# Kernel tuning notes

Measured on AMD Instinct MI355X. Metric: run time of the kernel, lower is better.

Reference implementation:

```python
import jax, jax.numpy as jnp
import numpy as np

N = 50000   # nodes
E = 800000  # edges
G = 64      # graphs in batch
D = 128     # num_input
H = 128     # num_hidden
O = 10      # num_output


def _linear_params(key, fan_in, fan_out):
    k1, k2 = jax.random.split(key)
    s = 1.0 / np.sqrt(fan_in)
    W = jax.random.uniform(k1, (fan_out, fan_in), jnp.float32, -s, s)
    b = jax.random.uniform(k2, (fan_out,), jnp.float32, -s, s)
    return W, b


def setup_inputs() -> dict:
    key = jax.random.key(0)
    ks = jax.random.split(key, 12)
    x = jax.random.normal(ks[0], (N, D), jnp.float32)
    edge_index = jax.random.randint(ks[1], (2, E), 0, N, dtype=jnp.int32).astype(jnp.int64)
    batch = jnp.sort(jax.random.randint(ks[2], (N,), 0, G, dtype=jnp.int32)).astype(jnp.int64)

    W_rel1, b_rel1 = _linear_params(ks[3], D, H)
    W_root1, _ = _linear_params(ks[4], D, H)
    W_rel2, b_rel2 = _linear_params(ks[5], H, H)
    W_root2, _ = _linear_params(ks[6], H, H)
    W_rel3, b_rel3 = _linear_params(ks[7], H, H)
    W_root3, _ = _linear_params(ks[8], H, H)
    W1, b1 = _linear_params(ks[9], 2 * H, 128)
    W2, b2 = _linear_params(ks[10], 128, 64)
    W3, b3 = _linear_params(ks[11], 64, O)

    return dict(x=x, edge_index=edge_index, batch=batch,
                W_rel1=W_rel1, b_rel1=b_rel1, W_root1=W_root1,
                W_rel2=W_rel2, b_rel2=b_rel2, W_root2=W_root2,
                W_rel3=W_rel3, b_rel3=b_rel3, W_root3=W_root3,
                W1=W1, b1=b1, W2=W2, b2=b2, W3=W3, b3=b3)


def _graph_conv(x, src, dst, W_rel, b_rel, W_root):
    # PyG GraphConv (aggr='add'): out_i = W_rel @ sum_{j->i} x_j + b_rel + W_root @ x_i
    agg = jax.ops.segment_sum(x[src], dst, num_segments=N)  # [N, d]
    return agg @ W_rel.T + b_rel + x @ W_root.T


def _pool(x, batch):
    # concat(global_max_pool, global_mean_pool) -> [G, 2d]
    mx = jax.ops.segment_max(x, batch, num_segments=G)
    mx = jnp.where(jnp.isfinite(mx), mx, 0.0)  # guard empty segments
    sm = jax.ops.segment_sum(x, batch, num_segments=G)
    cnt = jax.ops.segment_sum(jnp.ones((x.shape[0], 1), x.dtype), batch, num_segments=G)
    mean = sm / jnp.maximum(cnt, 1.0)
    return jnp.concatenate([mx, mean], axis=1)


def reference(x, edge_index, batch,
              W_rel1, b_rel1, W_root1,
              W_rel2, b_rel2, W_root2,
              W_rel3, b_rel3, W_root3,
              W1, b1, W2, b2, W3, b3):
    src, dst = edge_index[0], edge_index[1]
    h = jax.nn.relu(_graph_conv(x, src, dst, W_rel1, b_rel1, W_root1))
    x1 = _pool(h, batch)
    h = jax.nn.relu(_graph_conv(h, src, dst, W_rel2, b_rel2, W_root2))
    x2 = _pool(h, batch)
    h = jax.nn.relu(_graph_conv(h, src, dst, W_rel3, b_rel3, W_root3))
    x3 = _pool(h, batch)
    node_embs = h
    graph_emb = x1 + x2 + x3           # [G, 2H]
    z = jax.nn.relu(graph_emb @ W1.T + b1)
    z = jax.nn.relu(z @ W2.T + b2)     # dropout p=0 -> no-op
    logits = z @ W3.T + b3             # [G, O]
    return logits, node_embs, graph_emb
```

## Files before the change

kernel.cpp:

```cpp
#include <hip/hip_runtime.h>
#include <hip/hip_bf16.h>

#define NN 50000
#define EE 800000
#define GG 64
#define NBUCK 196
#define ABLOCKS 125
#define CHUNK 6400
#define BCAP 8192
#define SPANCAP 512
#define PARTN 3125
#define PSZ 400000

typedef __attribute__((ext_vector_type(8))) short bf16x8;
typedef __attribute__((ext_vector_type(4))) float f32x4;

__device__ __forceinline__ float bflo(unsigned u) { return __uint_as_float(u << 16); }
__device__ __forceinline__ float bfhi(unsigned u) { return __uint_as_float(u & 0xffff0000u); }
__device__ __forceinline__ float b2f(unsigned short s) { return __uint_as_float(((unsigned)s) << 16); }
__device__ __forceinline__ unsigned short f2bf(float f) {
    __hip_bfloat16 h = __float2bfloat16(f);
    union { __hip_bfloat16 h; unsigned short u; } cv; cv.h = h; return cv.u;
}

__global__ void detect_kernel(const unsigned* __restrict__ xw,
                              const unsigned* __restrict__ eiw,
                              int* __restrict__ flags) {
    __shared__ int s_cnt, s_nz;
    if (threadIdx.x == 0) { s_cnt = 0; s_nz = 0; }
    __syncthreads();
    int cnt = 0;
    for (int i = threadIdx.x; i < 4096; i += 256) {
        unsigned w = xw[(size_t)i * 711];
        unsigned elo = (w >> 7) & 0xFF;
        if (elo >= 100 && elo <= 140) cnt++;
    }
    int nz = 0;
    for (int i = threadIdx.x; i < 1024; i += 256) {
        unsigned w = eiw[(size_t)i * 1560 + 1];
        if (w != 0) nz++;
    }
    atomicAdd(&s_cnt, cnt);
    atomicAdd(&s_nz, nz);
    __syncthreads();
    if (threadIdx.x == 0) {
        flags[0] = (s_cnt < 3600) ? 1 : 0;
        flags[1] = (s_nz  < 8)    ? 1 : 0;
    }
}

struct WPtrs { const void* p[15]; };

__global__ __launch_bounds__(256) void prep_kernel(const void* __restrict__ xsrc,
                                                   const unsigned* __restrict__ eiw,
                                                   WPtrs wp,
                                                   unsigned short* __restrict__ arena,
                                                   int* __restrict__ counts,
                                                   uint4* __restrict__ zero_region,
                                                   const int* __restrict__ flags) {
    const int b = blockIdx.x;
    const int tid = threadIdx.x;
    const int isF32 = flags[0];

    if (b < 3125) {
        const int total4 = NN * 128 / 4;
        for (int i = b * 256 + tid; i < total4; i += 800000) {
            uint2 o;
            if (isF32) {
                float4 f = ((const float4*)xsrc)[i];
                o.x = (unsigned)f2bf(f.x) | ((unsigned)f2bf(f.y) << 16);
                o.y = (unsigned)f2bf(f.z) | ((unsigned)f2bf(f.w) << 16);
            } else {
                o = ((const uint2*)xsrc)[i];
            }
            ((uint2*)arena)[i] = o;
        }
    } else if (b < 3674) {
        const int cnt[15] = {16384,128,16384, 16384,128,16384, 16384,128,16384,
                             32768,128,8192,64,640,10};
        const int dst[15] = {19200000,19232768,19216384, 19232896,19265664,19249280,
                             19265792,19298560,19282176,
                             19298688,19331456,19331584,19339776,19339840,19340480};
        const int total = 140490;
        int i = (b - 3125) * 256 + tid;
        if (i < total) {
            int seg = 0, base = 0;
            while (i - base >= cnt[seg]) { base += cnt[seg]; ++seg; }
            int off = i - base;
            const void* s = wp.p[seg];
            arena[dst[seg] + off] =
                isF32 ? f2bf(((const float*)s)[off]) : ((const unsigned short*)s)[off];
        }
    } else if (b < 3799) {
        __shared__ int hist[256];
        hist[tid] = 0;
        __syncthreads();
        const int i64 = flags[1];
        const int e0 = (b - 3674) * CHUNK;
        for (int it = 0; it < CHUNK / 256; ++it) {
            int e = e0 + it * 256 + tid;
            int d = (int)(i64 ? eiw[(size_t)2 * (EE + e)] : eiw[EE + e]);
            atomicAdd(&hist[d >> 8], 1);
        }
        __syncthreads();
        counts[(b - 3674) * 256 + tid] = hist[tid];
    } else {
        zero_region[(b - 3799) * 256 + tid] = (uint4){0, 0, 0, 0};
    }
}

__global__ __launch_bounds__(256) void bucket_offsets(const int* __restrict__ counts,
                                                      int* __restrict__ offsets,
                                                      int* __restrict__ bucket_base) {
    __shared__ int s[256];
    const int t = threadIdx.x;
    int col = 0;
    for (int b = 0; b < ABLOCKS; ++b) col += counts[b * 256 + t];
    s[t] = col;
    __syncthreads();
    for (int d = 1; d < 256; d <<= 1) {
        int x = (t >= d) ? s[t - d] : 0;
        __syncthreads();
        s[t] += x;
        __syncthreads();
    }
    int base = s[t] - col;
    bucket_base[t] = base;
    if (t == 255) bucket_base[256] = s[255];
    int run = base;
    for (int b = 0; b < ABLOCKS; ++b) {
        offsets[b * 256 + t] = run;
        run += counts[b * 256 + t];
    }
}

__global__ __launch_bounds__(256) void bucket_scatter(const unsigned* __restrict__ eiw,
                                                      const int* __restrict__ offsets,
                                                      unsigned* __restrict__ packed,
                                                      const int* __restrict__ flags) {
    __shared__ int cur[256];
    cur[threadIdx.x] = offsets[blockIdx.x * 256 + threadIdx.x];
    __syncthreads();
    int i64 = flags[1];
    int e0 = blockIdx.x * CHUNK;
    for (int it = 0; it < CHUNK / 256; ++it) {
        int e = e0 + it * 256 + threadIdx.x;
        int s = (int)(i64 ? eiw[(size_t)2 * e]        : eiw[e]);
        int d = (int)(i64 ? eiw[(size_t)2 * (EE + e)] : eiw[EE + e]);
        int pos = atomicAdd(&cur[d >> 8], 1);
        packed[pos] = ((unsigned)s << 8) | (unsigned)(d & 255);
    }
}

__global__ __launch_bounds__(256) void bucket_sort(const unsigned* __restrict__ packed,
                                                   const int* __restrict__ bucket_base,
                                                   int* __restrict__ csr_src,
                                                   int* __restrict__ row_ptr) {
    __shared__ unsigned sbuf[BCAP];
    __shared__ int hist[256];
    __shared__ int cur[256];
    const int t = threadIdx.x;
    const int b = blockIdx.x;
    const int lo = bucket_base[b];
    int n = bucket_base[b + 1] - lo;
    if (n > BCAP) n = BCAP;

    hist[t] = 0;
    __syncthreads();
    for (int i = t; i < n; i += 256) {
        unsigned p = packed[lo + i];
        sbuf[i] = p;
        atomicAdd(&hist[p & 255], 1);
    }
    __syncthreads();
    int v = hist[t];
    __shared__ int s[256];
    s[t] = v;
    __syncthreads();
    for (int d = 1; d < 256; d <<= 1) {
        int x = (t >= d) ? s[t - d] : 0;
        __syncthreads();
        s[t] += x;
        __syncthreads();
    }
    int start = s[t] - v;
    int node = b * 256 + t;
    if (node < NN) row_ptr[node] = lo + start;
    if (b == 0 && t == 0) row_ptr[NN] = EE;
    cur[t] = start;
    __syncthreads();
    for (int i = t; i < n; i += 256) {
        unsigned p = sbuf[i];
        int pos = atomicAdd(&cur[p & 255], 1);
        csr_src[lo + pos] = (int)(p >> 8);
    }
}

__global__ __launch_bounds__(256, 8) void conv_fused(const unsigned short* __restrict__ hin,
                                                     const int* __restrict__ row_ptr,
                                                     const int* __restrict__ csr_src,
                                                     const unsigned short* __restrict__ Wrel,
                                                     const unsigned short* __restrict__ Wroot,
                                                     const unsigned short* __restrict__ brel,
                                                     const unsigned* __restrict__ bw,
                                                     unsigned* __restrict__ pmx,
                                                     float* __restrict__ psum,
                                                     float* __restrict__ ppart,
                                                     unsigned short* __restrict__ outb,
                                                     void* __restrict__ outG,
                                                     const int* __restrict__ flags) {
    __shared__ __align__(16) unsigned short tile[16][136];
    __shared__ int sbatch[16];
    __shared__ int s_rp[17];
    __shared__ int s_idx[SPANCAP];

    const int tid  = threadIdx.x;
    const int wv   = tid >> 6;
    const int lane = tid & 63;
    const int m0   = blockIdx.x * 16;

    if (tid < 17) s_rp[tid] = row_ptr[m0 + tid];
    if (tid >= 32 && tid < 48) {
        const int i64 = flags[1];
        int rr = m0 + (tid - 32);
        sbatch[tid - 32] = (int)(i64 ? bw[(size_t)2 * rr] : bw[rr]);
    }
    __syncthreads();
    const int base = s_rp[0];
    const int span = s_rp[16] - base;
    const int nst  = (span < SPANCAP) ? span : SPANCAP;
    for (int i = tid; i < nst; i += 256) s_idx[i] = csr_src[base + i];
    __syncthreads();

    const int qd  = lane >> 4;
    const int l16 = lane & 15;
    const int lr  = wv * 4 + qd;
    const int jb  = s_rp[lr]     - base;
    const int je  = s_rp[lr + 1] - base;
    const uint4* h16 = (const uint4*)hin;

    float a0 = 0.f, a1 = 0.f, a2 = 0.f, a3 = 0.f,
          a4 = 0.f, a5 = 0.f, a6 = 0.f, a7 = 0.f;

    if (span <= SPANCAP) {
        int j = jb;
        for (; j + 8 <= je; j += 8) {
            int idx[8];
            #pragma unroll
            for (int q = 0; q < 8; ++q) idx[q] = s_idx[j + q];
            uint4 u[8];
            #pragma unroll
            for (int q = 0; q < 8; ++q) u[q] = h16[(size_t)idx[q] * 16 + l16];
            #pragma unroll
            for (int q = 0; q < 8; ++q) {
                a0 += bflo(u[q].x); a1 += bfhi(u[q].x);
                a2 += bflo(u[q].y); a3 += bfhi(u[q].y);
                a4 += bflo(u[q].z); a5 += bfhi(u[q].z);
                a6 += bflo(u[q].w); a7 += bfhi(u[q].w);
            }
        }
        if (j < je) {
            #pragma unroll
            for (int q = 0; q < 8; ++q) {
                int ii = j + q;
                int ic = (ii < je - 1) ? ii : (je - 1);
                float sc = (ii < je) ? 1.f : 0.f;
                uint4 u = h16[(size_t)s_idx[ic] * 16 + l16];
                a0 = fmaf(bflo(u.x), sc, a0); a1 = fmaf(bfhi(u.x), sc, a1);
                a2 = fmaf(bflo(u.y), sc, a2); a3 = fmaf(bfhi(u.y), sc, a3);
                a4 = fmaf(bflo(u.z), sc, a4); a5 = fmaf(bfhi(u.z), sc, a5);
                a6 = fmaf(bflo(u.w), sc, a6); a7 = fmaf(bfhi(u.w), sc, a7);
            }
        }
    } else {
        for (int j = jb; j < je; j += 8) {
            #pragma unroll
            for (int q = 0; q < 8; ++q) {
                int ii = j + q;
                int ic = (ii < je - 1) ? ii : (je - 1);
                float sc = (ii < je) ? 1.f : 0.f;
                uint4 u = h16[(size_t)csr_src[base + ic] * 16 + l16];
                a0 = fmaf(bflo(u.x), sc, a0); a1 = fmaf(bfhi(u.x), sc, a1);
                a2 = fmaf(bflo(u.y), sc, a2); a3 = fmaf(bfhi(u.y), sc, a3);
                a4 = fmaf(bflo(u.z), sc, a4); a5 = fmaf(bfhi(u.z), sc, a5);
                a6 = fmaf(bflo(u.w), sc, a6); a7 = fmaf(bfhi(u.w), sc, a7);
            }
        }
    }

    {
        uint4 o;
        o.x = (unsigned)f2bf(a0) | ((unsigned)f2bf(a1) << 16);
        o.y = (unsigned)f2bf(a2) | ((unsigned)f2bf(a3) << 16);
        o.z = (unsigned)f2bf(a4) | ((unsigned)f2bf(a5) << 16);
        o.w = (unsigned)f2bf(a6) | ((unsigned)f2bf(a7) << 16);
        *(uint4*)&tile[lr][l16 * 8] = o;
    }
    __syncthreads();

    const int mrow = lane & 15;
    const int quad = lane >> 4;
    const int r    = m0 + mrow;

    f32x4 acc[2];
    acc[0] = (f32x4){0.f, 0.f, 0.f, 0.f};
    acc[1] = (f32x4){0.f, 0.f, 0.f, 0.f};

    #pragma unroll
    for (int kk = 0; kk < 8; ++kk) {
        const unsigned short* Bs = (kk < 4) ? Wrel : Wroot;
        const int kc = (kk & 3) * 32 + quad * 8;
        bf16x8 a;
        if (kk < 4) a = *(const bf16x8*)&tile[mrow][kc];
        else        a = *(const bf16x8*)(hin + (size_t)r * 128 + kc);
        #pragma unroll
        for (int n = 0; n < 2; ++n) {
            const int col0 = (wv * 2 + n) * 16;
            bf16x8 b = *(const bf16x8*)(Bs + (size_t)(col0 + mrow) * 128 + kc);
            acc[n] = __builtin_amdgcn_mfma_f32_16x16x32_bf16(a, b, acc[n], 0, 0, 0);
        }
    }

    __syncthreads();

    #pragma unroll
    for (int n = 0; n < 2; ++n) {
        const int col = (wv * 2 + n) * 16 + mrow;
        const float bias = b2f(brel[col]);
        #pragma unroll
        for (int i = 0; i < 4; ++i) {
            const int lrow = quad * 4 + i;
            float v = fmaxf(acc[n][i] + bias, 0.f);
            tile[lrow][col] = f2bf(v);
        }
    }
    __syncthreads();

    const int isF32 = flags[0];
    {
        const int lr2 = tid >> 4;
        const int c16 = tid & 15;
        uint4 v = *(const uint4*)&tile[lr2][c16 * 8];
        ((uint4*)outb)[(size_t)(m0 + lr2) * 16 + c16] = v;
        if (outG) {
            if (isF32) {
                float4* p = (float4*)outG + 160 + (size_t)(m0 + lr2) * 32 + c16 * 2;
                p[0] = (float4){bflo(v.x), bfhi(v.x), bflo(v.y), bfhi(v.y)};
                p[1] = (float4){bflo(v.z), bfhi(v.z), bflo(v.w), bfhi(v.w)};
            } else {
                uint4* p = (uint4*)((unsigned short*)outG + 640);
                p[(size_t)(m0 + lr2) * 16 + c16] = v;
            }
        }
    }

    if (tid < 128) {
        const int col = tid;
        const int slice = blockIdx.x & 7;
        int rr = 0;
        float mx = 0.f, sm = 0.f;
        if (ppart) {
            const int g0 = sbatch[0];
            for (; rr < 16 && sbatch[rr] == g0; ++rr) {
                float v = b2f(tile[rr][col]);
                mx = fmaxf(mx, v); sm += v;
            }
            ppart[(size_t)blockIdx.x * 128 + col] = mx;
            ppart[(size_t)PSZ + (size_t)blockIdx.x * 128 + col] = sm;
            mx = 0.f; sm = 0.f;
        }
        if (rr < 16) {
            int curg = sbatch[rr];
            for (; rr < 16; ++rr) {
                int g = sbatch[rr];
                if (g != curg) {
                    atomicMax(&pmx[(slice * GG + curg) * 128 + col], __float_as_uint(mx));
                    unsafeAtomicAdd(&psum[(slice * GG + curg) * 128 + col], sm);
                    curg = g; mx = 0.f; sm = 0.f;
                }
                float v = b2f(tile[rr][col]);
                mx = fmaxf(mx, v);
                sm += v;
            }
            atomicMax(&pmx[(slice * GG + curg) * 128 + col], __float_as_uint(mx));
            unsafeAtomicAdd(&psum[(slice * GG + curg) * 128 + col], sm);
        }
    }
}

__global__ __launch_bounds__(256) void mlp_kernel(const unsigned* __restrict__ pmxL,
                                                  const float* __restrict__ psum,
                                                  const float* __restrict__ part,
                                                  const unsigned* __restrict__ bw,
                                                  const unsigned short* __restrict__ W1,
                                                  const unsigned short* __restrict__ b1,
                                                  const unsigned short* __restrict__ W2,
                                                  const unsigned short* __restrict__ b2,
                                                  const unsigned short* __restrict__ W3,
                                                  const unsigned short* __restrict__ b3,
                                                  void* __restrict__ out,
                                                  const int* __restrict__ flags) {
    int g = blockIdx.x;
    int t = threadIdx.x;
    int isF32 = flags[0];
    int i64 = flags[1];
    __shared__ float sge[256];
    __shared__ float sz1[128];
    __shared__ float sz2[64];

    int lo = 0, hi = NN;
    while (lo < hi) {
        int mid = (lo + hi) >> 1;
        int bv = (int)(i64 ? bw[(size_t)2 * mid] : bw[mid]);
        if (bv < g) lo = mid + 1; else hi = mid;
    }
    int start = lo;
    hi = NN;
    while (lo < hi) {
        int mid = (lo + hi) >> 1;
        int bv = (int)(i64 ? bw[(size_t)2 * mid] : bw[mid]);
        if (bv < g + 1) lo = mid + 1; else hi = mid;
    }
    int cnt = lo - start;

    int b_lo = (start + 15) >> 4;
    int b_hi = (cnt > 0) ? ((start + cnt - 1) >> 4) : (b_lo - 1);

    float v;
    if (t < 128) {
        v = 0.f;
        #pragma unroll
        for (int L = 0; L < 3; ++L) {
            float m = 0.f;
            #pragma unroll
            for (int s = 0; s < 8; ++s)
                m = fmaxf(m, __uint_as_float(pmxL[((L * 8 + s) * GG + g) * 128 + t]));
            if (part) {
                const float* pm = part + (size_t)L * 2 * PSZ;
                for (int b = b_lo; b <= b_hi; ++b)
                    m = fmaxf(m, pm[(size_t)b * 128 + t]);
            }
            v += m;
        }
    } else {
        float sm = 0.f;
        #pragma unroll
        for (int s = 0; s < 8; ++s) sm += psum[(s * GG + g) * 128 + (t - 128)];
        if (part) {
            #pragma unroll
            for (int L = 0; L < 3; ++L) {
                const float* ps = part + (size_t)L * 2 * PSZ + PSZ;
                for (int b = b_lo; b <= b_hi; ++b)
                    sm += ps[(size_t)b * 128 + (t - 128)];
            }
        }
        v = sm / fmaxf((float)cnt, 1.f);
    }
    sge[t] = v;
    size_t geo = (size_t)640 + (size_t)NN * 128 + (size_t)g * 256 + t;
    if (isF32) ((float*)out)[geo] = v;
    else       ((unsigned short*)out)[geo] = f2bf(v);
    __syncthreads();

    if (t < 128) {
        float acc = b2f(b1[t]);
        for (int k = 0; k < 256; ++k) acc = fmaf(sge[k], b2f(W1[t * 256 + k]), acc);
        sz1[t] = fmaxf(acc, 0.f);
    }
    __syncthreads();
    if (t < 64) {
        float acc = b2f(b2[t]);
        for (int k = 0; k < 128; ++k) acc = fmaf(sz1[k], b2f(W2[t * 128 + k]), acc);
        sz2[t] = fmaxf(acc, 0.f);
    }
    __syncthreads();
    if (t < 10) {
        float acc = b2f(b3[t]);
        for (int k = 0; k < 64; ++k) acc = fmaf(sz2[k], b2f(W3[t * 64 + k]), acc);
        size_t o = (size_t)g * 10 + t;
        if (isF32) ((float*)out)[o] = acc;
        else       ((unsigned short*)out)[o] = f2bf(acc);
    }
}

#define XBF_OFF   0
#define HA_OFF    6400000
#define HB_OFF    12800000
#define WR1_OFF   19200000
#define WO1_OFF   19216384
#define BR1_OFF   19232768
#define WR2_OFF   19232896
#define WO2_OFF   19249280
#define BR2_OFF   19265664
#define WR3_OFF   19265792
#define WO3_OFF   19282176
#define BR3_OFF   19298560
#define W1_OFF    19298688
#define B1_OFF    19331456
#define W2_OFF    19331584
#define B2_OFF    19339776
#define W3_OFF    19339840
#define B3_OFF    19340480
#define ARENA_END 19340490

extern "C" void kernel_launch(void* const* d_in, const int* in_sizes, int n_in,
                              void* d_out, int out_size, void* d_ws, size_t ws_size,
                              hipStream_t stream) {
    unsigned short* arena = (unsigned short*)d_ws;
    size_t intBase = ((size_t)ARENA_END * 2 + 255) & ~(size_t)255;
    char* ib = (char*)d_ws + intBase;
    int*      row_ptr = (int*)ib;
    int*      csr_src = (int*)(ib + 200064);
    unsigned* packed  = (unsigned*)(ib + 3400064);
    int*      counts  = (int*)(ib + 6600064);
    int*      offsets = (int*)(ib + 6728064);
    int*      bbase   = (int*)(ib + 6856064);
    unsigned* pmxL    = (unsigned*)(ib + 6857344);
    float*    psum    = (float*)(ib + 7643776);
    int*      flags   = (int*)(ib + 7905920);
    float*    part    = (float*)(ib + 7906048);

    size_t need = intBase + 7906048 + (size_t)3 * 2 * PSZ * 4;
    float* partP = (ws_size >= need) ? part : nullptr;

    const unsigned* eiw = (const unsigned*)d_in[1];
    const unsigned* bw  = (const unsigned*)d_in[2];
    dim3 blk(256);

    detect_kernel<<<1, 256, 0, stream>>>((const unsigned*)d_in[0], eiw, flags);

    WPtrs wp;
    for (int i = 0; i < 15; ++i) wp.p[i] = d_in[3 + i];
    prep_kernel<<<4055, blk, 0, stream>>>(d_in[0], eiw, wp, arena, counts,
                                          (uint4*)pmxL, flags);

    bucket_offsets<<<1, blk, 0, stream>>>(counts, offsets, bbase);
    bucket_scatter<<<ABLOCKS, blk, 0, stream>>>(eiw, offsets, packed, flags);
    bucket_sort<<<NBUCK, blk, 0, stream>>>(packed, bbase, csr_src, row_ptr);

    const int convGrid = NN / 16;

    conv_fused<<<convGrid, blk, 0, stream>>>(arena + XBF_OFF, row_ptr, csr_src,
                                             arena + WR1_OFF, arena + WO1_OFF, arena + BR1_OFF,
                                             bw, pmxL, psum,
                                             partP ? partP : nullptr,
                                             arena + HA_OFF, nullptr, flags);
    conv_fused<<<convGrid, blk, 0, stream>>>(arena + HA_OFF, row_ptr, csr_src,
                                             arena + WR2_OFF, arena + WO2_OFF, arena + BR2_OFF,
                                             bw, pmxL + 65536, psum,
                                             partP ? partP + (size_t)2 * PSZ : nullptr,
                                             arena + HB_OFF, nullptr, flags);
    conv_fused<<<convGrid, blk, 0, stream>>>(arena + HB_OFF, row_ptr, csr_src,
                                             arena + WR3_OFF, arena + WO3_OFF, arena + BR3_OFF,
                                             bw, pmxL + 131072, psum,
                                             partP ? partP + (size_t)4 * PSZ : nullptr,
                                             arena + XBF_OFF, d_out, flags);

    mlp_kernel<<<GG, blk, 0, stream>>>(pmxL, psum, partP, bw,
                                       arena + W1_OFF, arena + B1_OFF,
                                       arena + W2_OFF, arena + B2_OFF,
                                       arena + W3_OFF, arena + B3_OFF, d_out, flags);
}
```

Baseline: 380.5 us.

## Shrink CSR indices to 16-bit, widen gather unroll, pack pool partials as bf16

Source indices in the CSR are stored as 16-bit values, which is valid because node ids stay below 65536. This halves index traffic and the shared-memory index buffer. The conv gather loop now issues 16 row loads per iteration instead of 8, the root-term rows are prefetched into registers before the barrier, and launch bounds drop from 8 to 4 blocks per CU to leave room for the extra registers. Per-block pool partials (max and sum) are packed as two bf16 values in one word, which halves that traffic at some cost in sum precision. Graph start offsets are computed once in the single-block offsets kernel, replacing the per-block binary searches in the MLP kernel, though that single block now also scans every node.

```diff
diff --git a/kernel.cpp b/kernel.cpp
--- a/kernel.cpp
+++ b/kernel.cpp
@@ -10,7 +10,6 @@
 #define BCAP 8192
 #define SPANCAP 512
 #define PARTN 3125
-#define PSZ 400000
 
 typedef __attribute__((ext_vector_type(8))) short bf16x8;
 typedef __attribute__((ext_vector_type(4))) float f32x4;
@@ -111,7 +110,10 @@
 
 __global__ __launch_bounds__(256) void bucket_offsets(const int* __restrict__ counts,
                                                       int* __restrict__ offsets,
-                                                      int* __restrict__ bucket_base) {
+                                                      int* __restrict__ bucket_base,
+                                                      const unsigned* __restrict__ bw,
+                                                      int* __restrict__ gstart,
+                                                      const int* __restrict__ flags) {
     __shared__ int s[256];
     const int t = threadIdx.x;
     int col = 0;
@@ -131,6 +133,14 @@
     for (int b = 0; b < ABLOCKS; ++b) {
         offsets[b * 256 + t] = run;
         run += counts[b * 256 + t];
+    }
+    if (t < 65) gstart[t] = NN;
+    __syncthreads();
+    const int i64 = flags[1];
+    for (int i = t; i < NN; i += 256) {
+        int g  = (int)(i64 ? bw[(size_t)2 * i] : bw[i]);
+        int gp = (i == 0) ? -1 : (int)(i64 ? bw[(size_t)2 * (i - 1)] : bw[i - 1]);
+        for (int gg = gp + 1; gg <= g; ++gg) gstart[gg] = i;
     }
 }
 
@@ -154,7 +164,7 @@
 
 __global__ __launch_bounds__(256) void bucket_sort(const unsigned* __restrict__ packed,
                                                    const int* __restrict__ bucket_base,
-                                                   int* __restrict__ csr_src,
+                                                   unsigned short* __restrict__ csr_src,
                                                    int* __restrict__ row_ptr) {
     __shared__ unsigned sbuf[BCAP];
     __shared__ int hist[256];
@@ -192,32 +202,34 @@
     for (int i = t; i < n; i += 256) {
         unsigned p = sbuf[i];
         int pos = atomicAdd(&cur[p & 255], 1);
-        csr_src[lo + pos] = (int)(p >> 8);
-    }
-}
-
-__global__ __launch_bounds__(256, 8) void conv_fused(const unsigned short* __restrict__ hin,
+        csr_src[lo + pos] = (unsigned short)(p >> 8);
+    }
+}
+
+__global__ __launch_bounds__(256, 4) void conv_fused(const unsigned short* __restrict__ hin,
                                                      const int* __restrict__ row_ptr,
-                                                     const int* __restrict__ csr_src,
+                                                     const unsigned short* __restrict__ csr16,
                                                      const unsigned short* __restrict__ Wrel,
                                                      const unsigned short* __restrict__ Wroot,
                                                      const unsigned short* __restrict__ brel,
                                                      const unsigned* __restrict__ bw,
                                                      unsigned* __restrict__ pmx,
                                                      float* __restrict__ psum,
-                                                     float* __restrict__ ppart,
+                                                     unsigned* __restrict__ ppart,
                                                      unsigned short* __restrict__ outb,
                                                      void* __restrict__ outG,
                                                      const int* __restrict__ flags) {
     __shared__ __align__(16) unsigned short tile[16][136];
     __shared__ int sbatch[16];
     __shared__ int s_rp[17];
-    __shared__ int s_idx[SPANCAP];
+    __shared__ unsigned short s_idx[SPANCAP];
 
     const int tid  = threadIdx.x;
     const int wv   = tid >> 6;
     const int lane = tid & 63;
     const int m0   = blockIdx.x * 16;
+    const int mrow = lane & 15;
+    const int quad = lane >> 4;
 
     if (tid < 17) s_rp[tid] = row_ptr[m0 + tid];
     if (tid >= 32 && tid < 48) {
@@ -229,7 +241,13 @@
     const int base = s_rp[0];
     const int span = s_rp[16] - base;
     const int nst  = (span < SPANCAP) ? span : SPANCAP;
-    for (int i = tid; i < nst; i += 256) s_idx[i] = csr_src[base + i];
+    for (int i = tid; i < nst; i += 256) s_idx[i] = csr16[base + i];
+
+    bf16x8 rootv[4];
+    #pragma unroll
+    for (int k2 = 0; k2 < 4; ++k2)
+        rootv[k2] = *(const bf16x8*)(hin + (size_t)(m0 + mrow) * 128 + k2 * 32 + quad * 8);
+
     __syncthreads();
 
     const int qd  = lane >> 4;
@@ -244,7 +262,22 @@
 
     if (span <= SPANCAP) {
         int j = jb;
-        for (; j + 8 <= je; j += 8) {
+        for (; j + 16 <= je; j += 16) {
+            int idx[16];
+            #pragma unroll
+            for (int q = 0; q < 16; ++q) idx[q] = s_idx[j + q];
+            uint4 u[16];
+            #pragma unroll
+            for (int q = 0; q < 16; ++q) u[q] = h16[(size_t)idx[q] * 16 + l16];
+            #pragma unroll
+            for (int q = 0; q < 16; ++q) {
+                a0 += bflo(u[q].x); a1 += bfhi(u[q].x);
+                a2 += bflo(u[q].y); a3 += bfhi(u[q].y);
+                a4 += bflo(u[q].z); a5 += bfhi(u[q].z);
+                a6 += bflo(u[q].w); a7 += bfhi(u[q].w);
+            }
+        }
+        if (j + 8 <= je) {
             int idx[8];
             #pragma unroll
             for (int q = 0; q < 8; ++q) idx[q] = s_idx[j + q];
@@ -258,6 +291,7 @@
                 a4 += bflo(u[q].z); a5 += bfhi(u[q].z);
                 a6 += bflo(u[q].w); a7 += bfhi(u[q].w);
             }
+            j += 8;
         }
         if (j < je) {
             #pragma unroll
@@ -279,7 +313,7 @@
                 int ii = j + q;
                 int ic = (ii < je - 1) ? ii : (je - 1);
                 float sc = (ii < je) ? 1.f : 0.f;
-                uint4 u = h16[(size_t)csr_src[base + ic] * 16 + l16];
+                uint4 u = h16[(size_t)csr16[base + ic] * 16 + l16];
                 a0 = fmaf(bflo(u.x), sc, a0); a1 = fmaf(bfhi(u.x), sc, a1);
                 a2 = fmaf(bflo(u.y), sc, a2); a3 = fmaf(bfhi(u.y), sc, a3);
                 a4 = fmaf(bflo(u.z), sc, a4); a5 = fmaf(bfhi(u.z), sc, a5);
@@ -298,10 +332,6 @@
     }
     __syncthreads();
 
-    const int mrow = lane & 15;
-    const int quad = lane >> 4;
-    const int r    = m0 + mrow;
-
     f32x4 acc[2];
     acc[0] = (f32x4){0.f, 0.f, 0.f, 0.f};
     acc[1] = (f32x4){0.f, 0.f, 0.f, 0.f};
@@ -312,7 +342,7 @@
         const int kc = (kk & 3) * 32 + quad * 8;
         bf16x8 a;
         if (kk < 4) a = *(const bf16x8*)&tile[mrow][kc];
-        else        a = *(const bf16x8*)(hin + (size_t)r * 128 + kc);
+        else        a = rootv[kk - 4];
         #pragma unroll
         for (int n = 0; n < 2; ++n) {
             const int col0 = (wv * 2 + n) * 16;
@@ -365,8 +395,8 @@
                 float v = b2f(tile[rr][col]);
                 mx = fmaxf(mx, v); sm += v;
             }
-            ppart[(size_t)blockIdx.x * 128 + col] = mx;
-            ppart[(size_t)PSZ + (size_t)blockIdx.x * 128 + col] = sm;
+            ppart[(size_t)blockIdx.x * 128 + col] =
+                (unsigned)f2bf(mx) | ((unsigned)f2bf(sm) << 16);
             mx = 0.f; sm = 0.f;
         }
         if (rr < 16) {
@@ -390,8 +420,8 @@
 
 __global__ __launch_bounds__(256) void mlp_kernel(const unsigned* __restrict__ pmxL,
                                                   const float* __restrict__ psum,
-                                                  const float* __restrict__ part,
-                                                  const unsigned* __restrict__ bw,
+                                                  const unsigned* __restrict__ part,
+                                                  const int* __restrict__ gstart,
                                                   const unsigned short* __restrict__ W1,
                                                   const unsigned short* __restrict__ b1,
                                                   const unsigned short* __restrict__ W2,
@@ -403,28 +433,16 @@
     int g = blockIdx.x;
     int t = threadIdx.x;
     int isF32 = flags[0];
-    int i64 = flags[1];
     __shared__ float sge[256];
     __shared__ float sz1[128];
     __shared__ float sz2[64];
 
-    int lo = 0, hi = NN;
-    while (lo < hi) {
-        int mid = (lo + hi) >> 1;
-        int bv = (int)(i64 ? bw[(size_t)2 * mid] : bw[mid]);
-        if (bv < g) lo = mid + 1; else hi = mid;
-    }
-    int start = lo;
-    hi = NN;
-    while (lo < hi) {
-        int mid = (lo + hi) >> 1;
-        int bv = (int)(i64 ? bw[(size_t)2 * mid] : bw[mid]);
-        if (bv < g + 1) lo = mid + 1; else hi = mid;
-    }
-    int cnt = lo - start;
+    int start = gstart[g];
+    int end   = gstart[g + 1];
+    int cnt   = end - start;
 
     int b_lo = (start + 15) >> 4;
-    int b_hi = (cnt > 0) ? ((start + cnt - 1) >> 4) : (b_lo - 1);
+    int b_hi = (cnt > 0) ? ((end - 1) >> 4) : (b_lo - 1);
 
     float v;
     if (t < 128) {
@@ -436,9 +454,9 @@
             for (int s = 0; s < 8; ++s)
                 m = fmaxf(m, __uint_as_float(pmxL[((L * 8 + s) * GG + g) * 128 + t]));
             if (part) {
-                const float* pm = part + (size_t)L * 2 * PSZ;
+                const unsigned* pm = part + (size_t)L * PARTN * 128;
                 for (int b = b_lo; b <= b_hi; ++b)
-                    m = fmaxf(m, pm[(size_t)b * 128 + t]);
+                    m = fmaxf(m, b2f((unsigned short)(pm[(size_t)b * 128 + t] & 0xffffu)));
             }
             v += m;
         }
@@ -449,9 +467,9 @@
         if (part) {
             #pragma unroll
             for (int L = 0; L < 3; ++L) {
-                const float* ps = part + (size_t)L * 2 * PSZ + PSZ;
+                const unsigned* pm = part + (size_t)L * PARTN * 128;
                 for (int b = b_lo; b <= b_hi; ++b)
-                    sm += ps[(size_t)b * 128 + (t - 128)];
+                    sm += b2f((unsigned short)(pm[(size_t)b * 128 + (t - 128)] >> 16));
             }
         }
         v = sm / fmaxf((float)cnt, 1.f);
@@ -509,19 +527,20 @@
     unsigned short* arena = (unsigned short*)d_ws;
     size_t intBase = ((size_t)ARENA_END * 2 + 255) & ~(size_t)255;
     char* ib = (char*)d_ws + intBase;
-    int*      row_ptr = (int*)ib;
-    int*      csr_src = (int*)(ib + 200064);
-    unsigned* packed  = (unsigned*)(ib + 3400064);
-    int*      counts  = (int*)(ib + 6600064);
-    int*      offsets = (int*)(ib + 6728064);
-    int*      bbase   = (int*)(ib + 6856064);
-    unsigned* pmxL    = (unsigned*)(ib + 6857344);
-    float*    psum    = (float*)(ib + 7643776);
-    int*      flags   = (int*)(ib + 7905920);
-    float*    part    = (float*)(ib + 7906048);
-
-    size_t need = intBase + 7906048 + (size_t)3 * 2 * PSZ * 4;
-    float* partP = (ws_size >= need) ? part : nullptr;
+    int*            row_ptr = (int*)ib;
+    unsigned short* csr_src = (unsigned short*)(ib + 200064);
+    unsigned*       packed  = (unsigned*)(ib + 1800064);
+    int*            counts  = (int*)(ib + 5000064);
+    int*            offsets = (int*)(ib + 5128064);
+    int*            bbase   = (int*)(ib + 5256064);
+    unsigned*       pmxL    = (unsigned*)(ib + 5257216);
+    float*          psum    = (float*)(ib + 6043648);
+    int*            flags   = (int*)(ib + 6305792);
+    int*            gstart  = (int*)(ib + 6305920);
+    unsigned*       part    = (unsigned*)(ib + 6306304);
+
+    size_t need = intBase + 6306304 + (size_t)3 * PARTN * 128 * 4;
+    unsigned* partP = (ws_size >= need) ? part : nullptr;
 
     const unsigned* eiw = (const unsigned*)d_in[1];
     const unsigned* bw  = (const unsigned*)d_in[2];
@@ -534,7 +553,7 @@
     prep_kernel<<<4055, blk, 0, stream>>>(d_in[0], eiw, wp, arena, counts,
                                           (uint4*)pmxL, flags);
 
-    bucket_offsets<<<1, blk, 0, stream>>>(counts, offsets, bbase);
+    bucket_offsets<<<1, blk, 0, stream>>>(counts, offsets, bbase, bw, gstart, flags);
     bucket_scatter<<<ABLOCKS, blk, 0, stream>>>(eiw, offsets, packed, flags);
     bucket_sort<<<NBUCK, blk, 0, stream>>>(packed, bbase, csr_src, row_ptr);
 
@@ -543,20 +562,20 @@
     conv_fused<<<convGrid, blk, 0, stream>>>(arena + XBF_OFF, row_ptr, csr_src,
                                              arena + WR1_OFF, arena + WO1_OFF, arena + BR1_OFF,
                                              bw, pmxL, psum,
-                                             partP ? partP : nullptr,
+                                             partP,
                                              arena + HA_OFF, nullptr, flags);
     conv_fused<<<convGrid, blk, 0, stream>>>(arena + HA_OFF, row_ptr, csr_src,
                                              arena + WR2_OFF, arena + WO2_OFF, arena + BR2_OFF,
                                              bw, pmxL + 65536, psum,
-                                             partP ? partP + (size_t)2 * PSZ : nullptr,
+                                             partP ? partP + (size_t)PARTN * 128 : nullptr,
                                              arena + HB_OFF, nullptr, flags);
     conv_fused<<<convGrid, blk, 0, stream>>>(arena + HB_OFF, row_ptr, csr_src,
                                              arena + WR3_OFF, arena + WO3_OFF, arena + BR3_OFF,
                                              bw, pmxL + 131072, psum,
-                                             partP ? partP + (size_t)4 * PSZ : nullptr,
+                                             partP ? partP + (size_t)2 * PARTN * 128 : nullptr,
                                              arena + XBF_OFF, d_out, flags);
 
-    mlp_kernel<<<GG, blk, 0, stream>>>(pmxL, psum, partP, bw,
+    mlp_kernel<<<GG, blk, 0, stream>>>(pmxL, psum, partP, gstart,
                                        arena + W1_OFF, arena + B1_OFF,
                                        arena + W2_OFF, arena + B2_OFF,
                                        arena + W3_OFF, arena + B3_OFF, d_out, flags);
```

Result: slower. 405.4 us (+6.5%).
